# Kernel tuning notes

Measured on AMD Instinct MI355X. Metric: run time of the kernel, lower is better.

The kernel has to match this reference:

```python
import jax, jax.numpy as jnp
import numpy as np

B, L, D_MODEL = 2, 2048, 1024
NH, FD = 16, 16            # num_heads, feature_dim
HD = D_MODEL // NH         # head_dim = 64
EPS = 1e-12


def taylor_exp(x):
    """2nd-order Taylor feature map of exp(q.k/sqrt(d)): phi(x)=[1, x/rrd, (x (x) x)/(rd*sqrt(2))].
    x: (b, h, l, d) -> (b, h, l, 1 + d + d*d)"""
    d = x.shape[-1]
    rd = np.sqrt(float(d))
    rrd = np.sqrt(rd)
    r2 = np.sqrt(2.0)
    x2 = (x[..., :, None] * x[..., None, :]).reshape(x.shape[:-1] + (d * d,)) / (rd * r2)
    ones = jnp.ones(x.shape[:-1] + (1,), dtype=x.dtype)
    return jnp.concatenate([ones, x / rrd, x2], axis=-1)


def setup_inputs() -> dict:
    key = jax.random.key(0)
    ks = jax.random.split(key, 5)
    x = jax.random.normal(ks[0], (B, L, D_MODEL), dtype=jnp.float32)
    s = 0.02  # small init scale keeps feature-map magnitudes sane
    Wq = jax.random.normal(ks[1], (D_MODEL, NH * FD), dtype=jnp.float32) * s
    Wk = jax.random.normal(ks[2], (D_MODEL, NH * FD), dtype=jnp.float32) * s
    Wv = jax.random.normal(ks[3], (D_MODEL, NH * HD), dtype=jnp.float32) * s
    Wo = jax.random.normal(ks[4], (NH * HD, D_MODEL), dtype=jnp.float32) * s
    return {"x": x, "Wq": Wq, "Wk": Wk, "Wv": Wv, "Wo": Wo}


def reference(x, Wq, Wk, Wv, Wo):
    b, l, _ = x.shape
    # projections, split heads: (b, h, l, d)
    q = (x @ Wq).reshape(b, l, NH, FD).transpose(0, 2, 1, 3)
    k = (x @ Wk).reshape(b, l, NH, FD).transpose(0, 2, 1, 3)
    v = (x @ Wv).reshape(b, l, NH, HD).transpose(0, 2, 1, 3)
    qf = taylor_exp(q)  # (b, h, l, D) with D = 1 + FD + FD^2 = 273
    kf = taylor_exp(k)
    # causal quadratic view of linear attention (parallel training form)
    A = jnp.einsum('bhnd,bhmd->bhnm', qf, kf)
    A = jnp.tril(A)
    y = jnp.einsum('bhnm,bhme->bhne', A, v)
    # denominator: q_feat . cumsum(k_feat)
    z = 1.0 / (jnp.einsum('bhld,bhld->bhl', qf, jnp.cumsum(kf, axis=2)) + EPS)
    y = y * z[..., None]
    y = y.transpose(0, 2, 1, 3).reshape(b, l, NH * HD)
    return y @ Wo
```

## Files before the change

### kernel.cpp

```cpp
#include <hip/hip_runtime.h>

#define LL 2048
#define NH 16
#define DFEAT 273
#define SROW 320
#define EPSV 1e-12f
#define INV_RRD 0.5f
#define INV_Q 0.17677669529663687f

#define OFF_Q  ((size_t)0)
#define OFF_K  ((size_t)1048576)
#define OFF_VT ((size_t)2097152)
#define OFF_S  ((size_t)4194304)
#define OFF_ZK ((size_t)14680064)
#define OFF_Y  ((size_t)15007744)

typedef __attribute__((ext_vector_type(8))) _Float16 f16x8;
typedef __attribute__((ext_vector_type(4))) float f32x4;

#define MFMAH(a, b, c) __builtin_amdgcn_mfma_f32_16x16x32_f16(a, b, c, 0, 0, 0)

__device__ __forceinline__ void llds16(const _Float16* g, _Float16* s) {
  __builtin_amdgcn_global_load_lds(
      (const __attribute__((address_space(1))) short*)(const short*)g,
      (__attribute__((address_space(3))) short*)(short*)s, 16, 0, 0);
}

__device__ __forceinline__ float featv(const float (*m)[17], int c, int d) {
  if (d == 0) return 1.f;
  if (d < 17) return m[c][d - 1] * INV_RRD;
  if (d < DFEAT) { int d2 = d - 17; return m[c][d2 >> 4] * m[c][d2 & 15] * INV_Q; }
  return 0.f;
}

__global__ __launch_bounds__(256) void xcvt_kernel(const float* __restrict__ x,
                                                   _Float16* __restrict__ xf) {
  int i = (blockIdx.x * 256 + threadIdx.x) * 8;
  float4 a = *(const float4*)&x[i];
  float4 b = *(const float4*)&x[i + 4];
  f16x8 o;
  o[0] = (_Float16)a.x; o[1] = (_Float16)a.y; o[2] = (_Float16)a.z;
  o[3] = (_Float16)a.w; o[4] = (_Float16)b.x; o[5] = (_Float16)b.y;
  o[6] = (_Float16)b.z; o[7] = (_Float16)b.w;
  *(f16x8*)&xf[i] = o;
}

__global__ __launch_bounds__(256) void tcvt_qkv_kernel(
    const float* __restrict__ Wq, const float* __restrict__ Wk,
    const float* __restrict__ Wv, _Float16* __restrict__ dst) {
  __shared__ float tile[32][33];
  const int k0 = blockIdx.x * 32, n0 = blockIdx.y * 32;
  const float* src; int ncol, c0;
  if (n0 < 256)      { src = Wq; ncol = 256;  c0 = n0; }
  else if (n0 < 512) { src = Wk; ncol = 256;  c0 = n0 - 256; }
  else               { src = Wv; ncol = 1024; c0 = n0 - 512; }
  const int t = threadIdx.x;
  {
    int kk = t >> 3, c4 = (t & 7) * 4;
    float4 v = *(const float4*)&src[(size_t)(k0 + kk) * ncol + c0 + c4];
    tile[kk][c4] = v.x; tile[kk][c4 + 1] = v.y;
    tile[kk][c4 + 2] = v.z; tile[kk][c4 + 3] = v.w;
  }
  __syncthreads();
  int cc = t >> 3, k4 = (t & 7) * 4;
  union { unsigned long long u; _Float16 f[4]; } p;
  p.f[0] = (_Float16)tile[k4 + 0][cc];
  p.f[1] = (_Float16)tile[k4 + 1][cc];
  p.f[2] = (_Float16)tile[k4 + 2][cc];
  p.f[3] = (_Float16)tile[k4 + 3][cc];
  *(unsigned long long*)&dst[(size_t)(n0 + cc) * 1024 + k0 + k4] = p.u;
}

__global__ __launch_bounds__(256) void tcvt_wo_kernel(
    const float* __restrict__ Wo, _Float16* __restrict__ dst) {
  __shared__ float tile[32][33];
  const int k0 = blockIdx.x * 32, n0 = blockIdx.y * 32;
  const int t = threadIdx.x;
  {
    int kk = t >> 3, c4 = (t & 7) * 4;
    float4 v = *(const float4*)&Wo[(size_t)(k0 + kk) * 1024 + n0 + c4];
    tile[kk][c4] = v.x; tile[kk][c4 + 1] = v.y;
    tile[kk][c4 + 2] = v.z; tile[kk][c4 + 3] = v.w;
  }
  __syncthreads();
  int cc = t >> 3, k4 = (t & 7) * 4;
  union { unsigned long long u; _Float16 f[4]; } p;
  p.f[0] = (_Float16)tile[k4 + 0][cc];
  p.f[1] = (_Float16)tile[k4 + 1][cc];
  p.f[2] = (_Float16)tile[k4 + 2][cc];
  p.f[3] = (_Float16)tile[k4 + 3][cc];
  *(unsigned long long*)&dst[(size_t)(n0 + cc) * 1024 + k0 + k4] = p.u;
}

template <int MODE>
__global__ __launch_bounds__(256) void bgemm_kernel(
    const _Float16* __restrict__ A, const _Float16* __restrict__ B,
    float* __restrict__ dst, _Float16* __restrict__ vT) {
  __shared__ _Float16 lds[12288];
  const int t = threadIdx.x;
  const int w = t >> 6, l = t & 63;
  const int m0 = blockIdx.y * 128, n0 = blockIdx.x * 64;
  const int rsub = l >> 3;
  const int g8 = ((l & 7) ^ rsub) * 8;
  const int fr = l & 15, ks = l >> 4;
  const int wr = w >> 1, wc = w & 1;

  f32x4 acc[4][2];
#pragma unroll
  for (int i = 0; i < 4; i++)
#pragma unroll
    for (int j = 0; j < 2; j++) acc[i][j] = (f32x4){0.f, 0.f, 0.f, 0.f};

  for (int k0 = 0; k0 < 1024; k0 += 64) {
#pragma unroll
    for (int j = 0; j < 4; j++) {
      const int c = w * 4 + j;
      llds16(A + (size_t)(m0 + c * 8 + rsub) * 1024 + k0 + g8, &lds[c * 512]);
    }
#pragma unroll
    for (int j = 0; j < 2; j++) {
      const int c = w * 2 + j;
      llds16(B + (size_t)(n0 + c * 8 + rsub) * 1024 + k0 + g8,
             &lds[8192 + c * 512]);
    }
    __syncthreads();
#pragma unroll
    for (int kk = 0; kk < 2; kk++) {
      const int so = ((kk * 4 + ks) ^ (fr & 7)) * 8;
      f16x8 fa[4], fb[2];
#pragma unroll
      for (int mi = 0; mi < 4; mi++)
        fa[mi] = *(const f16x8*)&lds[(wr * 64 + mi * 16 + fr) * 64 + so];
#pragma unroll
      for (int ni = 0; ni < 2; ni++)
        fb[ni] = *(const f16x8*)&lds[8192 + (wc * 32 + ni * 16 + fr) * 64 + so];
#pragma unroll
      for (int mi = 0; mi < 4; mi++)
#pragma unroll
        for (int ni = 0; ni < 2; ni++)
          acc[mi][ni] = MFMAH(fa[mi], fb[ni], acc[mi][ni]);
    }
    __syncthreads();
  }

  const int bb = m0 >> 11;
#pragma unroll
  for (int mi = 0; mi < 4; mi++) {
    const int lrow = (m0 & (LL - 1)) + wr * 64 + mi * 16 + ks * 4;
    const int grow = m0 + wr * 64 + mi * 16 + ks * 4;
#pragma unroll
    for (int ni = 0; ni < 2; ni++) {
      const int cn = n0 + wc * 32 + ni * 16 + fr;
      if (MODE == 1) {
#pragma unroll
        for (int r = 0; r < 4; r++)
          dst[(size_t)(grow + r) * 1024 + cn] = acc[mi][ni][r];
      } else if (cn < 256) {
        const int hq = cn >> 4, f = cn & 15;
#pragma unroll
        for (int r = 0; r < 4; r++)
          dst[OFF_Q + ((size_t)(bb * NH + hq) * LL + lrow + r) * 16 + f] =
              acc[mi][ni][r];
      } else if (cn < 512) {
        const int c2 = cn - 256, hq = c2 >> 4, f = c2 & 15;
#pragma unroll
        for (int r = 0; r < 4; r++)
          dst[OFF_K + ((size_t)(bb * NH + hq) * LL + lrow + r) * 16 + f] =
              acc[mi][ni][r];
      } else {
        const int c2 = cn - 512, hh = c2 >> 6, e = c2 & 63;
        union { unsigned long long u; _Float16 f[4]; } p;
#pragma unroll
        for (int r = 0; r < 4; r++) p.f[r] = (_Float16)acc[mi][ni][r];
        *(unsigned long long*)&vT[((size_t)(bb * NH + hh) * 64 + e) * LL +
                                  lrow] = p.u;
      }
    }
  }
}

__global__ __launch_bounds__(256) void chunk_state_kernel(
    float* __restrict__ ws, const _Float16* __restrict__ vT) {
  __shared__ float kc[64][17];
  __shared__ _Float16 vt[4096];
  const int t = threadIdx.x, blk = blockIdx.x;
  const int bh = blk >> 5, nc = blk & 31;
  const int w = t >> 6, l = t & 63;
  const int rsub = l >> 3, g8 = ((l & 7) ^ rsub) * 8;
  const int fr = l & 15, ks = l >> 4;

  {
    int c = t >> 2, u = (t & 3) * 4;
    float4 v =
        *(const float4*)&ws[OFF_K + ((size_t)bh * LL + nc * 64 + c) * 16 + u];
    kc[c][u] = v.x; kc[c][u + 1] = v.y; kc[c][u + 2] = v.z; kc[c][u + 3] = v.w;
  }
  const _Float16* vg = vT + (size_t)bh * 64 * LL + nc * 64;
#pragma unroll
  for (int j = 0; j < 2; j++) {
    const int c = w * 2 + j;
    llds16(vg + (size_t)(c * 8 + rsub) * LL + g8, &vt[c * 512]);
  }
  __syncthreads();

  _Float16* S16 = (_Float16*)(ws + OFF_S) + (size_t)blk * (64 * SROW);
  float* zk = ws + OFF_ZK + (size_t)blk * SROW;

  for (int t5 = 0; t5 < 5; t5++) {
    const int d0 = t5 * 64;
    const int d = d0 + w * 16 + fr;
    f16x8 af[2];
    float zpart = 0.f;
#pragma unroll
    for (int kk = 0; kk < 2; kk++)
#pragma unroll
      for (int j = 0; j < 8; j++) {
        float v = featv(kc, kk * 32 + ks * 8 + j, d);
        zpart += v;
        af[kk][j] = (_Float16)v;
      }
    zpart += __shfl_xor(zpart, 16);
    zpart += __shfl_xor(zpart, 32);
    if (ks == 0 && d < DFEAT) zk[d] = zpart;

    f32x4 sacc[4];
#pragma unroll
    for (int i = 0; i < 4; i++) sacc[i] = (f32x4){0.f, 0.f, 0.f, 0.f};
#pragma unroll
    for (int ni = 0; ni < 4; ni++)
#pragma unroll
      for (int kk = 0; kk < 2; kk++) {
        f16x8 fb = *(const f16x8*)&vt[(ni * 16 + fr) * 64 +
                                      (((kk * 4 + ks)) ^ (fr & 7)) * 8];
        sacc[ni] = MFMAH(af[kk], fb, sacc[ni]);
      }
    const int dstart = d0 + w * 16 + ks * 4;
#pragma unroll
    for (int ni = 0; ni < 4; ni++) {
      union { unsigned long long u; _Float16 f[4]; } p;
#pragma unroll
      for (int r = 0; r < 4; r++)
        p.f[r] = (dstart + r < DFEAT) ? (_Float16)sacc[ni][r] : (_Float16)0.f;
      *(unsigned long long*)&S16[(size_t)(ni * 16 + fr) * SROW + dstart] = p.u;
    }
  }
}

__global__ __launch_bounds__(256) void scan_kernel(float* __restrict__ ws) {
  const int bh = blockIdx.y;
  const int E = blockIdx.x * 256 + threadIdx.x;
  const int SU = 64 * SROW / 2;
  if (E < SU) {
    unsigned int* base =
        (unsigned int*)((_Float16*)(ws + OFF_S) + (size_t)bh * 32 * (64 * SROW)) +
        E;
    float r0 = 0.f, r1 = 0.f;
    for (int nc = 0; nc < 32; nc++) {
      union { unsigned int u; _Float16 f[2]; } in, ov;
      in.u = base[(size_t)nc * SU];
      float v0 = (float)in.f[0], v1 = (float)in.f[1];
      ov.f[0] = (_Float16)r0; ov.f[1] = (_Float16)r1;
      base[(size_t)nc * SU] = ov.u;
      r0 += v0; r1 += v1;
    }
  } else if (E < SU + SROW) {
    float* base = ws + OFF_ZK + (size_t)bh * 32 * SROW + (E - SU);
    float run = 0.f;
    for (int nc = 0; nc < 32; nc++) {
      float v = base[(size_t)nc * SROW];
      base[(size_t)nc * SROW] = run;
      run += v;
    }
  }
}

__global__ __launch_bounds__(256) void chunk_out_kernel(
    float* __restrict__ ws, const _Float16* __restrict__ vT,
    _Float16* __restrict__ y) {
  __shared__ float qc[64][17], kc[64][17];
  __shared__ _Float16 vt[4096], sp[4096];
  __shared__ float zpf[64];
  __shared__ float zinv[64];
  const int t = threadIdx.x, blk = blockIdx.x;
  const int bh = blk >> 5, nc = blk & 31;
  const int bb = bh >> 4, h = bh & 15;
  const int w = t >> 6, l = t & 63;
  const int rsub = l >> 3, g8 = ((l & 7) ^ rsub) * 8;
  const int fr = l & 15, ks = l >> 4;
  const int crowA = w * 16 + fr;

  {
    int c = t >> 2, u = (t & 3) * 4;
    float4 v =
        *(const float4*)&ws[OFF_Q + ((size_t)bh * LL + nc * 64 + c) * 16 + u];
    qc[c][u] = v.x; qc[c][u + 1] = v.y; qc[c][u + 2] = v.z; qc[c][u + 3] = v.w;
    float4 s =
        *(const float4*)&ws[OFF_K + ((size_t)bh * LL + nc * 64 + c) * 16 + u];
    kc[c][u] = s.x; kc[c][u + 1] = s.y; kc[c][u + 2] = s.z; kc[c][u + 3] = s.w;
  }
  const _Float16* vg = vT + (size_t)bh * 64 * LL + nc * 64;
#pragma unroll
  for (int j = 0; j < 2; j++) {
    const int c = w * 2 + j;
    llds16(vg + (size_t)(c * 8 + rsub) * LL + g8, &vt[c * 512]);
  }

  const _Float16* Sp16 =
      (const _Float16*)(ws + OFF_S) + (size_t)blk * (64 * SROW);
  const float* zp = ws + OFF_ZK + (size_t)blk * SROW;

  f32x4 acc[4];
#pragma unroll
  for (int i = 0; i < 4; i++) acc[i] = (f32x4){0.f, 0.f, 0.f, 0.f};
  float zrow = 0.f;

  for (int t5 = 0; t5 < 5; t5++) {
    const int d0 = t5 * 64;
#pragma unroll
    for (int j = 0; j < 2; j++) {
      const int c = w * 2 + j;
      llds16(Sp16 + (size_t)(c * 8 + rsub) * SROW + d0 + g8, &sp[c * 512]);
    }
    if (t < 64) zpf[t] = (d0 + t < DFEAT) ? zp[d0 + t] : 0.f;
    __syncthreads();
    f16x8 af[2];
#pragma unroll
    for (int kk = 0; kk < 2; kk++)
#pragma unroll
      for (int j = 0; j < 8; j++) {
        const int dd = kk * 32 + ks * 8 + j;
        float v = featv(qc, crowA, d0 + dd);
        zrow = fmaf(v, zpf[dd], zrow);
        af[kk][j] = (_Float16)v;
      }
#pragma unroll
    for (int ni = 0; ni < 4; ni++)
#pragma unroll
      for (int kk = 0; kk < 2; kk++) {
        f16x8 fb = *(const f16x8*)&sp[(ni * 16 + fr) * 64 +
                                      (((kk * 4 + ks)) ^ (fr & 7)) * 8];
        acc[ni] = MFMAH(af[kk], fb, acc[ni]);
      }
    __syncthreads();
  }

  {
    float qreg[16];
#pragma unroll
    for (int i = 0; i < 16; i++) qreg[i] = qc[crowA][i];
    f16x8 aq;
#pragma unroll
    for (int j = 0; j < 8; j++)
      aq[j] = (ks < 2) ? (_Float16)(0.25f * qreg[(ks * 8 + j) & 15])
                       : (_Float16)0.f;
    const f32x4 zero4 = {0.f, 0.f, 0.f, 0.f};
    f32x4 sD[4];
#pragma unroll
    for (int ni = 0; ni < 4; ni++) {
      f16x8 bk;
#pragma unroll
      for (int j = 0; j < 8; j++)
        bk[j] = (ks < 2) ? (_Float16)kc[ni * 16 + fr][(ks * 8 + j) & 15]
                         : (_Float16)0.f;
      sD[ni] = MFMAH(aq, bk, zero4);
    }
#pragma unroll
    for (int ni = 0; ni < 4; ni++) {
      const int cp = ni * 16 + fr;
#pragma unroll
      for (int r = 0; r < 4; r++) {
        const int ci = w * 16 + ks * 4 + r;
        float s = sD[ni][r];
        float f = 1.f + s + 0.5f * s * s;
        f = (cp <= ci) ? f : 0.f;
        sp[ci * 64 + (((cp >> 3) ^ (ci & 7)) * 8) + (cp & 7)] = (_Float16)f;
      }
    }
  }
  __syncthreads();
  {
    f16x8 ff[2];
#pragma unroll
    for (int kk = 0; kk < 2; kk++) {
      ff[kk] = *(const f16x8*)&sp[crowA * 64 +
                                  (((kk * 4 + ks)) ^ (fr & 7)) * 8];
#pragma unroll
      for (int j = 0; j < 8; j++) zrow += (float)ff[kk][j];
    }
#pragma unroll
    for (int ni = 0; ni < 4; ni++)
#pragma unroll
      for (int kk = 0; kk < 2; kk++) {
        f16x8 fb = *(const f16x8*)&vt[(ni * 16 + fr) * 64 +
                                      (((kk * 4 + ks)) ^ (fr & 7)) * 8];
        acc[ni] = MFMAH(ff[kk], fb, acc[ni]);
      }
  }
  zrow += __shfl_xor(zrow, 16);
  zrow += __shfl_xor(zrow, 32);
  if (ks == 0) zinv[crowA] = 1.f / (zrow + EPSV);
  __syncthreads();

  const int crow = w * 16 + ks * 4;
#pragma unroll
  for (int ni = 0; ni < 4; ni++) {
    const int e = ni * 16 + fr;
#pragma unroll
    for (int r = 0; r < 4; r++) {
      float v = acc[ni][r] * zinv[crow + r];
      y[((size_t)bb * LL + nc * 64 + crow + r) * 1024 + h * 64 + e] =
          (_Float16)v;
    }
  }
}

extern "C" void kernel_launch(void* const* d_in, const int* in_sizes, int n_in,
                              void* d_out, int out_size, void* d_ws,
                              size_t ws_size, hipStream_t stream) {
  (void)in_sizes; (void)n_in; (void)out_size; (void)ws_size;
  const float* x  = (const float*)d_in[0];
  const float* Wq = (const float*)d_in[1];
  const float* Wk = (const float*)d_in[2];
  const float* Wv = (const float*)d_in[3];
  const float* Wo = (const float*)d_in[4];
  float* ws = (float*)d_ws;
  float* out = (float*)d_out;

  _Float16* vT = (_Float16*)(ws + OFF_VT);
  _Float16* y16 = (_Float16*)(ws + OFF_Y);
  _Float16* xf = (_Float16*)(ws + OFF_S);
  _Float16* BT = xf + (size_t)4096 * 1024;
  _Float16* WoT = (_Float16*)(ws + OFF_Q);

  xcvt_kernel<<<2048, 256, 0, stream>>>(x, xf);
  tcvt_qkv_kernel<<<dim3(32, 48), 256, 0, stream>>>(Wq, Wk, Wv, BT);
  bgemm_kernel<0><<<dim3(24, 32), 256, 0, stream>>>(xf, BT, ws, vT);
  chunk_state_kernel<<<1024, 256, 0, stream>>>(ws, vT);
  scan_kernel<<<dim3(42, 32), 256, 0, stream>>>(ws);
  chunk_out_kernel<<<1024, 256, 0, stream>>>(ws, vT, y16);
  tcvt_wo_kernel<<<dim3(32, 32), 256, 0, stream>>>(Wo, WoT);
  bgemm_kernel<1><<<dim3(16, 32), 256, 0, stream>>>(y16, WoT, out, nullptr);
}
```

Baseline: 170.3 us.

## Fuse prep kernels, double-buffer GEMM and chunk-out LDS, shrink state row padding

Merges the x conversion and the three weight transpose kernels into one prep launch, with Wo moved to its own workspace region. The GEMM and chunk_out kernels now double-buffer their LDS tiles so the next global-to-LDS load overlaps the current MFMAs. The chunk state row stride drops from 320 to 280 to cut scan and state traffic, and the scan loop is unrolled by four to batch its loads. The risks are more LDS use per block, which can lower occupancy, and a possible missing barrier between stages. Reads of the padded state columns past 280 in the last d-chunk also need checking.

Measured after the change: 160.9 us. 1.06x faster.

```diff
diff --git a/kernel.cpp b/kernel.cpp
--- a/kernel.cpp
+++ b/kernel.cpp
@@ -3,17 +3,18 @@
 #define LL 2048
 #define NH 16
 #define DFEAT 273
-#define SROW 320
+#define SROW 280
 #define EPSV 1e-12f
 #define INV_RRD 0.5f
 #define INV_Q 0.17677669529663687f
 
-#define OFF_Q  ((size_t)0)
-#define OFF_K  ((size_t)1048576)
-#define OFF_VT ((size_t)2097152)
-#define OFF_S  ((size_t)4194304)
-#define OFF_ZK ((size_t)14680064)
-#define OFF_Y  ((size_t)15007744)
+#define OFF_Q   ((size_t)0)
+#define OFF_K   ((size_t)1048576)
+#define OFF_VT  ((size_t)2097152)
+#define OFF_S   ((size_t)4194304)
+#define OFF_ZK  ((size_t)13369408)
+#define OFF_Y   ((size_t)13656128)
+#define OFF_WOT ((size_t)15753280)
 
 typedef __attribute__((ext_vector_type(8))) _Float16 f16x8;
 typedef __attribute__((ext_vector_type(4))) float f32x4;
@@ -33,28 +34,43 @@
   return 0.f;
 }
 
-__global__ __launch_bounds__(256) void xcvt_kernel(const float* __restrict__ x,
-                                                   _Float16* __restrict__ xf) {
-  int i = (blockIdx.x * 256 + threadIdx.x) * 8;
-  float4 a = *(const float4*)&x[i];
-  float4 b = *(const float4*)&x[i + 4];
-  f16x8 o;
-  o[0] = (_Float16)a.x; o[1] = (_Float16)a.y; o[2] = (_Float16)a.z;
-  o[3] = (_Float16)a.w; o[4] = (_Float16)b.x; o[5] = (_Float16)b.y;
-  o[6] = (_Float16)b.z; o[7] = (_Float16)b.w;
-  *(f16x8*)&xf[i] = o;
-}
-
-__global__ __launch_bounds__(256) void tcvt_qkv_kernel(
-    const float* __restrict__ Wq, const float* __restrict__ Wk,
-    const float* __restrict__ Wv, _Float16* __restrict__ dst) {
+__global__ __launch_bounds__(256) void prep_kernel(
+    const float* __restrict__ x, const float* __restrict__ Wq,
+    const float* __restrict__ Wk, const float* __restrict__ Wv,
+    const float* __restrict__ Wo, _Float16* __restrict__ xf,
+    _Float16* __restrict__ BT, _Float16* __restrict__ WoT) {
   __shared__ float tile[32][33];
-  const int k0 = blockIdx.x * 32, n0 = blockIdx.y * 32;
-  const float* src; int ncol, c0;
-  if (n0 < 256)      { src = Wq; ncol = 256;  c0 = n0; }
-  else if (n0 < 512) { src = Wk; ncol = 256;  c0 = n0 - 256; }
-  else               { src = Wv; ncol = 1024; c0 = n0 - 512; }
+  const int bid = blockIdx.x;
   const int t = threadIdx.x;
+  if (bid < 2048) {
+    int i = (bid * 256 + t) * 8;
+    float4 a = *(const float4*)&x[i];
+    float4 b = *(const float4*)&x[i + 4];
+    f16x8 o;
+    o[0] = (_Float16)a.x; o[1] = (_Float16)a.y; o[2] = (_Float16)a.z;
+    o[3] = (_Float16)a.w; o[4] = (_Float16)b.x; o[5] = (_Float16)b.y;
+    o[6] = (_Float16)b.z; o[7] = (_Float16)b.w;
+    *(f16x8*)&xf[i] = o;
+    return;
+  }
+  const float* src;
+  _Float16* dst;
+  int ncol, c0, k0, n0;
+  if (bid < 3584) {
+    const int idx = bid - 2048;
+    k0 = (idx & 31) * 32;
+    n0 = (idx >> 5) * 32;
+    if (n0 < 256)      { src = Wq; ncol = 256;  c0 = n0; }
+    else if (n0 < 512) { src = Wk; ncol = 256;  c0 = n0 - 256; }
+    else               { src = Wv; ncol = 1024; c0 = n0 - 512; }
+    dst = BT;
+  } else {
+    const int idx = bid - 3584;
+    k0 = (idx & 31) * 32;
+    n0 = (idx >> 5) * 32;
+    src = Wo; ncol = 1024; c0 = n0;
+    dst = WoT;
+  }
   {
     int kk = t >> 3, c4 = (t & 7) * 4;
     float4 v = *(const float4*)&src[(size_t)(k0 + kk) * ncol + c0 + c4];
@@ -71,32 +87,11 @@
   *(unsigned long long*)&dst[(size_t)(n0 + cc) * 1024 + k0 + k4] = p.u;
 }
 
-__global__ __launch_bounds__(256) void tcvt_wo_kernel(
-    const float* __restrict__ Wo, _Float16* __restrict__ dst) {
-  __shared__ float tile[32][33];
-  const int k0 = blockIdx.x * 32, n0 = blockIdx.y * 32;
-  const int t = threadIdx.x;
-  {
-    int kk = t >> 3, c4 = (t & 7) * 4;
-    float4 v = *(const float4*)&Wo[(size_t)(k0 + kk) * 1024 + n0 + c4];
-    tile[kk][c4] = v.x; tile[kk][c4 + 1] = v.y;
-    tile[kk][c4 + 2] = v.z; tile[kk][c4 + 3] = v.w;
-  }
-  __syncthreads();
-  int cc = t >> 3, k4 = (t & 7) * 4;
-  union { unsigned long long u; _Float16 f[4]; } p;
-  p.f[0] = (_Float16)tile[k4 + 0][cc];
-  p.f[1] = (_Float16)tile[k4 + 1][cc];
-  p.f[2] = (_Float16)tile[k4 + 2][cc];
-  p.f[3] = (_Float16)tile[k4 + 3][cc];
-  *(unsigned long long*)&dst[(size_t)(n0 + cc) * 1024 + k0 + k4] = p.u;
-}
-
 template <int MODE>
 __global__ __launch_bounds__(256) void bgemm_kernel(
     const _Float16* __restrict__ A, const _Float16* __restrict__ B,
     float* __restrict__ dst, _Float16* __restrict__ vT) {
-  __shared__ _Float16 lds[12288];
+  __shared__ _Float16 lds[2][12288];
   const int t = threadIdx.x;
   const int w = t >> 6, l = t & 63;
   const int m0 = blockIdx.y * 128, n0 = blockIdx.x * 64;
@@ -111,29 +106,37 @@
 #pragma unroll
     for (int j = 0; j < 2; j++) acc[i][j] = (f32x4){0.f, 0.f, 0.f, 0.f};
 
-  for (int k0 = 0; k0 < 1024; k0 += 64) {
+  auto stage = [&](int buf, int k0) {
 #pragma unroll
     for (int j = 0; j < 4; j++) {
       const int c = w * 4 + j;
-      llds16(A + (size_t)(m0 + c * 8 + rsub) * 1024 + k0 + g8, &lds[c * 512]);
+      llds16(A + (size_t)(m0 + c * 8 + rsub) * 1024 + k0 + g8,
+             &lds[buf][c * 512]);
     }
 #pragma unroll
     for (int j = 0; j < 2; j++) {
       const int c = w * 2 + j;
       llds16(B + (size_t)(n0 + c * 8 + rsub) * 1024 + k0 + g8,
-             &lds[8192 + c * 512]);
-    }
-    __syncthreads();
+             &lds[buf][8192 + c * 512]);
+    }
+  };
+
+  stage(0, 0);
+  __syncthreads();
+  for (int tt = 0; tt < 16; ++tt) {
+    const int cur = tt & 1;
+    if (tt < 15) stage(cur ^ 1, (tt + 1) * 64);
 #pragma unroll
     for (int kk = 0; kk < 2; kk++) {
       const int so = ((kk * 4 + ks) ^ (fr & 7)) * 8;
       f16x8 fa[4], fb[2];
 #pragma unroll
       for (int mi = 0; mi < 4; mi++)
-        fa[mi] = *(const f16x8*)&lds[(wr * 64 + mi * 16 + fr) * 64 + so];
+        fa[mi] = *(const f16x8*)&lds[cur][(wr * 64 + mi * 16 + fr) * 64 + so];
 #pragma unroll
       for (int ni = 0; ni < 2; ni++)
-        fb[ni] = *(const f16x8*)&lds[8192 + (wc * 32 + ni * 16 + fr) * 64 + so];
+        fb[ni] =
+            *(const f16x8*)&lds[cur][8192 + (wc * 32 + ni * 16 + fr) * 64 + so];
 #pragma unroll
       for (int mi = 0; mi < 4; mi++)
 #pragma unroll
@@ -235,13 +238,16 @@
         sacc[ni] = MFMAH(af[kk], fb, sacc[ni]);
       }
     const int dstart = d0 + w * 16 + ks * 4;
-#pragma unroll
-    for (int ni = 0; ni < 4; ni++) {
-      union { unsigned long long u; _Float16 f[4]; } p;
-#pragma unroll
-      for (int r = 0; r < 4; r++)
-        p.f[r] = (dstart + r < DFEAT) ? (_Float16)sacc[ni][r] : (_Float16)0.f;
-      *(unsigned long long*)&S16[(size_t)(ni * 16 + fr) * SROW + dstart] = p.u;
+    if (dstart < SROW) {
+#pragma unroll
+      for (int ni = 0; ni < 4; ni++) {
+        union { unsigned long long u; _Float16 f[4]; } p;
+#pragma unroll
+        for (int r = 0; r < 4; r++)
+          p.f[r] = (dstart + r < DFEAT) ? (_Float16)sacc[ni][r] : (_Float16)0.f;
+        *(unsigned long long*)&S16[(size_t)(ni * 16 + fr) * SROW + dstart] =
+            p.u;
+      }
     }
   }
 }
@@ -255,21 +261,36 @@
         (unsigned int*)((_Float16*)(ws + OFF_S) + (size_t)bh * 32 * (64 * SROW)) +
         E;
     float r0 = 0.f, r1 = 0.f;
-    for (int nc = 0; nc < 32; nc++) {
-      union { unsigned int u; _Float16 f[2]; } in, ov;
-      in.u = base[(size_t)nc * SU];
-      float v0 = (float)in.f[0], v1 = (float)in.f[1];
-      ov.f[0] = (_Float16)r0; ov.f[1] = (_Float16)r1;
-      base[(size_t)nc * SU] = ov.u;
-      r0 += v0; r1 += v1;
+    for (int nc = 0; nc < 32; nc += 4) {
+      unsigned int av[4];
+      av[0] = base[(size_t)(nc + 0) * SU];
+      av[1] = base[(size_t)(nc + 1) * SU];
+      av[2] = base[(size_t)(nc + 2) * SU];
+      av[3] = base[(size_t)(nc + 3) * SU];
+#pragma unroll
+      for (int j = 0; j < 4; j++) {
+        union { unsigned int u; _Float16 f[2]; } in, ov;
+        in.u = av[j];
+        ov.f[0] = (_Float16)r0; ov.f[1] = (_Float16)r1;
+        base[(size_t)(nc + j) * SU] = ov.u;
+        r0 += (float)in.f[0];
+        r1 += (float)in.f[1];
+      }
     }
   } else if (E < SU + SROW) {
     float* base = ws + OFF_ZK + (size_t)bh * 32 * SROW + (E - SU);
     float run = 0.f;
-    for (int nc = 0; nc < 32; nc++) {
-      float v = base[(size_t)nc * SROW];
-      base[(size_t)nc * SROW] = run;
-      run += v;
+    for (int nc = 0; nc < 32; nc += 4) {
+      float av[4];
+      av[0] = base[(size_t)(nc + 0) * SROW];
+      av[1] = base[(size_t)(nc + 1) * SROW];
+      av[2] = base[(size_t)(nc + 2) * SROW];
+      av[3] = base[(size_t)(nc + 3) * SROW];
+#pragma unroll
+      for (int j = 0; j < 4; j++) {
+        base[(size_t)(nc + j) * SROW] = run;
+        run += av[j];
+      }
     }
   }
 }
@@ -278,8 +299,9 @@
     float* __restrict__ ws, const _Float16* __restrict__ vT,
     _Float16* __restrict__ y) {
   __shared__ float qc[64][17], kc[64][17];
-  __shared__ _Float16 vt[4096], sp[4096];
-  __shared__ float zpf[64];
+  __shared__ _Float16 vt[4096];
+  __shared__ _Float16 sp[2][4096];
+  __shared__ float zpf[2][64];
   __shared__ float zinv[64];
   const int t = threadIdx.x, blk = blockIdx.x;
   const int bh = blk >> 5, nc = blk & 31;
@@ -309,20 +331,32 @@
       (const _Float16*)(ws + OFF_S) + (size_t)blk * (64 * SROW);
   const float* zp = ws + OFF_ZK + (size_t)blk * SROW;
 
+  auto stage_sp = [&](int buf, int d0) {
+#pragma unroll
+    for (int j = 0; j < 2; j++) {
+      const int c = w * 2 + j;
+      llds16(Sp16 + (size_t)(c * 8 + rsub) * SROW + d0 + g8,
+             &sp[buf][c * 512]);
+    }
+  };
+
   f32x4 acc[4];
 #pragma unroll
   for (int i = 0; i < 4; i++) acc[i] = (f32x4){0.f, 0.f, 0.f, 0.f};
   float zrow = 0.f;
 
+  stage_sp(0, 0);
+  if (t < 64) zpf[0][t] = (t < DFEAT) ? zp[t] : 0.f;
+  __syncthreads();
+
   for (int t5 = 0; t5 < 5; t5++) {
     const int d0 = t5 * 64;
-#pragma unroll
-    for (int j = 0; j < 2; j++) {
-      const int c = w * 2 + j;
-      llds16(Sp16 + (size_t)(c * 8 + rsub) * SROW + d0 + g8, &sp[c * 512]);
-    }
-    if (t < 64) zpf[t] = (d0 + t < DFEAT) ? zp[d0 + t] : 0.f;
-    __syncthreads();
+    const int cur = t5 & 1;
+    if (t5 < 4) {
+      stage_sp(cur ^ 1, d0 + 64);
+      if (t < 64)
+        zpf[cur ^ 1][t] = (d0 + 64 + t < DFEAT) ? zp[d0 + 64 + t] : 0.f;
+    }
     f16x8 af[2];
 #pragma unroll
     for (int kk = 0; kk < 2; kk++)
@@ -330,15 +364,15 @@
       for (int j = 0; j < 8; j++) {
         const int dd = kk * 32 + ks * 8 + j;
         float v = featv(qc, crowA, d0 + dd);
-        zrow = fmaf(v, zpf[dd], zrow);
+        zrow = fmaf(v, zpf[cur][dd], zrow);
         af[kk][j] = (_Float16)v;
       }
 #pragma unroll
     for (int ni = 0; ni < 4; ni++)
 #pragma unroll
       for (int kk = 0; kk < 2; kk++) {
-        f16x8 fb = *(const f16x8*)&sp[(ni * 16 + fr) * 64 +
-                                      (((kk * 4 + ks)) ^ (fr & 7)) * 8];
+        f16x8 fb = *(const f16x8*)&sp[cur][(ni * 16 + fr) * 64 +
+                                          (((kk * 4 + ks)) ^ (fr & 7)) * 8];
         acc[ni] = MFMAH(af[kk], fb, acc[ni]);
       }
     __syncthreads();
@@ -373,7 +407,7 @@
         float s = sD[ni][r];
         float f = 1.f + s + 0.5f * s * s;
         f = (cp <= ci) ? f : 0.f;
-        sp[ci * 64 + (((cp >> 3) ^ (ci & 7)) * 8) + (cp & 7)] = (_Float16)f;
+        sp[0][ci * 64 + (((cp >> 3) ^ (ci & 7)) * 8) + (cp & 7)] = (_Float16)f;
       }
     }
   }
@@ -382,8 +416,8 @@
     f16x8 ff[2];
 #pragma unroll
     for (int kk = 0; kk < 2; kk++) {
-      ff[kk] = *(const f16x8*)&sp[crowA * 64 +
-                                  (((kk * 4 + ks)) ^ (fr & 7)) * 8];
+      ff[kk] = *(const f16x8*)&sp[0][crowA * 64 +
+                                     (((kk * 4 + ks)) ^ (fr & 7)) * 8];
 #pragma unroll
       for (int j = 0; j < 8; j++) zrow += (float)ff[kk][j];
     }
@@ -428,16 +462,14 @@
 
   _Float16* vT = (_Float16*)(ws + OFF_VT);
   _Float16* y16 = (_Float16*)(ws + OFF_Y);
+  _Float16* WoT = (_Float16*)(ws + OFF_WOT);
   _Float16* xf = (_Float16*)(ws + OFF_S);
   _Float16* BT = xf + (size_t)4096 * 1024;
-  _Float16* WoT = (_Float16*)(ws + OFF_Q);
-
-  xcvt_kernel<<<2048, 256, 0, stream>>>(x, xf);
-  tcvt_qkv_kernel<<<dim3(32, 48), 256, 0, stream>>>(Wq, Wk, Wv, BT);
+
+  prep_kernel<<<4608, 256, 0, stream>>>(x, Wq, Wk, Wv, Wo, xf, BT, WoT);
   bgemm_kernel<0><<<dim3(24, 32), 256, 0, stream>>>(xf, BT, ws, vT);
   chunk_state_kernel<<<1024, 256, 0, stream>>>(ws, vT);
-  scan_kernel<<<dim3(42, 32), 256, 0, stream>>>(ws);
+  scan_kernel<<<dim3(37, 32), 256, 0, stream>>>(ws);
   chunk_out_kernel<<<1024, 256, 0, stream>>>(ws, vT, y16);
-  tcvt_wo_kernel<<<dim3(32, 32), 256, 0, stream>>>(Wo, WoT);
   bgemm_kernel<1><<<dim3(16, 32), 256, 0, stream>>>(y16, WoT, out, nullptr);
 }
```
